# Optimization experiments

Hardware: AMD Instinct MI355X
Metric: run time of the kernel (lower is better)

The kernel has to match this reference:

```python
import jax, jax.numpy as jnp
import numpy as np

B, N, H = 16, 1024, 1024


def setup_inputs() -> dict:
    key = jax.random.key(0)
    ks = jax.random.split(key, 12)
    inv = 1.0 / np.sqrt(H)
    inp = {
        "x": jax.random.normal(ks[0], (B, N, H), jnp.float32),
        "atom_graph": jax.random.normal(ks[1], (B, N, N), jnp.float32),
        "variable_graph": jax.random.normal(ks[2], (B, N, N), jnp.float32),
        "Wq": jax.random.uniform(ks[3], (H, H), jnp.float32, -inv, inv),
        "bq": jax.random.uniform(ks[4], (H,), jnp.float32, -inv, inv),
        "Wk": jax.random.uniform(ks[5], (H, H), jnp.float32, -inv, inv),
        "bk": jax.random.uniform(ks[6], (H,), jnp.float32, -inv, inv),
        "Wv": jax.random.uniform(ks[7], (H, H), jnp.float32, -inv, inv),
        "bv": jax.random.uniform(ks[8], (H,), jnp.float32, -inv, inv),
        "predicate_pos": jax.random.randint(ks[9], (B, N), 0, 2, jnp.int32),
        "variable_tags": jax.random.randint(ks[10], (B, N), 0, 4, jnp.int32),
    }
    return inp


def _path_pool(h, predicate_pos):
    # h: [B,N,H]; predicate_pos: [B,N] in {0,1}
    b, n, d = h.shape
    i = jnp.arange(n)
    # pos[i-2] (value irrelevant for i<2, those branches handled explicitly)
    pp2 = jnp.pad(predicate_pos, ((0, 0), (2, 0)))[:, :n]  # [B,N]
    # window [s, e): i==0 -> [0,2); i==1 -> [0,3); pos[i-2]==1 -> [i,i+2); else [i-1,i+2)
    s = jnp.where(i < 2, 0, jnp.where(pp2 == 1, i, i - 1))  # [B,N]
    e = jnp.where(i == 0, 2, jnp.where(i == 1, 3, i + 2))    # [N]
    e = jnp.minimum(e, n)
    e = jnp.broadcast_to(e, (b, n))
    # prefix sums along node dim with a leading zero row -> windowed means via gather
    cs = jnp.concatenate([jnp.zeros((b, 1, d), h.dtype), jnp.cumsum(h, axis=1)], axis=1)  # [B,N+1,H]
    win_sum = (jnp.take_along_axis(cs, e[:, :, None], axis=1)
               - jnp.take_along_axis(cs, s[:, :, None], axis=1))  # [B,N,H]
    means = win_sum / (e - s)[:, :, None].astype(h.dtype)
    mask = (predicate_pos == 1).astype(h.dtype)  # [B,N]
    item = (means * mask[:, :, None]).sum(axis=1) / mask.sum(axis=1)[:, None]  # [B,H]
    return jnp.broadcast_to(item[:, None, :], (b, n, d))


def reference(x, atom_graph, variable_graph, Wq, bq, Wk, bk, Wv, bv,
              predicate_pos, variable_tags):
    scale = x.shape[-1] ** (-0.5)
    q = (x @ Wq.T + bq) * scale
    k = x @ Wk.T + bk
    v = x @ Wv.T + bv
    att = jnp.einsum("bnh,bmh->bnm", q, k) + atom_graph + variable_graph
    att = jax.nn.softmax(att, axis=-1)  # dropout is identity in eval
    h = jnp.einsum("bnm,bmh->bnh", att, v)
    return _path_pool(h, predicate_pos)
```

## Files before the change

kernel.cpp:

```cpp
#include <hip/hip_runtime.h>
#include <hip/hip_bf16.h>

#define BATCH 16
#define SEQ   1024
#define DIM   1024

typedef __attribute__((ext_vector_type(8))) short bf16x8;
typedef __attribute__((ext_vector_type(4))) float f32x4;
typedef __attribute__((ext_vector_type(4))) unsigned short us4;

__device__ __forceinline__ float bfu2f(unsigned short u) {
  union { unsigned int i; float f; } c; c.i = ((unsigned int)u) << 16; return c.f;
}
__device__ __forceinline__ unsigned short f2bfu(float f) {
  union { float f; unsigned int i; } c; c.f = f;
  return (unsigned short)((c.i + 0x7FFFu + ((c.i >> 16) & 1u)) >> 16);
}
__device__ __forceinline__ void async16(void* lds, const void* g) {
  __builtin_amdgcn_global_load_lds(
      (const __attribute__((address_space(1))) unsigned int*)g,
      (__attribute__((address_space(3))) unsigned int*)lds, 16, 0, 0);
}

__global__ void cast_f32_bf16(const float* __restrict__ in,
                              unsigned short* __restrict__ out, int n4) {
  int i = blockIdx.x * blockDim.x + threadIdx.x;
  if (i >= n4) return;
  f32x4 v = ((const f32x4*)in)[i];
  us4 o;
  o[0] = f2bfu(v[0]); o[1] = f2bfu(v[1]); o[2] = f2bfu(v[2]); o[3] = f2bfu(v[3]);
  ((us4*)out)[i] = o;
}

__global__ void castT_kernel(const float* __restrict__ Wq, const float* __restrict__ Wk,
                             unsigned short* __restrict__ WqT,
                             unsigned short* __restrict__ WkT) {
  const float* in = (blockIdx.z == 0) ? Wq : Wk;
  unsigned short* out = (blockIdx.z == 0) ? WqT : WkT;
  __shared__ float t[64][65];
  const int h0 = blockIdx.x * 64, i0 = blockIdx.y * 64;
  const int tid = threadIdx.x;
  const int sub = tid >> 4, c4 = tid & 15;
#pragma unroll
  for (int p = 0; p < 4; ++p) {
    const int row = p * 16 + sub;
    f32x4 v = *(const f32x4*)(in + (size_t)(h0 + row) * DIM + i0 + c4 * 4);
    t[row][c4 * 4 + 0] = v[0]; t[row][c4 * 4 + 1] = v[1];
    t[row][c4 * 4 + 2] = v[2]; t[row][c4 * 4 + 3] = v[3];
  }
  __syncthreads();
#pragma unroll
  for (int p = 0; p < 4; ++p) {
    const int orow = p * 16 + sub;
    us4 o;
    o[0] = f2bfu(t[c4 * 4 + 0][orow]);
    o[1] = f2bfu(t[c4 * 4 + 1][orow]);
    o[2] = f2bfu(t[c4 * 4 + 2][orow]);
    o[3] = f2bfu(t[c4 * 4 + 3][orow]);
    *(us4*)(out + (size_t)(i0 + orow) * DIM + h0 + c4 * 4) = o;
  }
}

__global__ void t12_kernel(const unsigned short* __restrict__ WqT,
                           const unsigned short* __restrict__ WkT,
                           const float* __restrict__ bq, const float* __restrict__ bk,
                           float* __restrict__ t1, float* __restrict__ t2) {
  const int y = blockIdx.y;
  const unsigned short* Wt = y ? WkT : WqT;
  const float* vec = y ? bq : bk;
  float* tout = y ? t2 : t1;
  const int wave = threadIdx.x >> 6, lane = threadIdx.x & 63;
  const int i = blockIdx.x * 4 + wave;
  const us4* wr = (const us4*)(Wt + (size_t)i * DIM);
  float s = 0.f;
#pragma unroll
  for (int t = 0; t < 4; ++t) {
    us4 w4 = wr[lane + 64 * t];
    f32x4 b4 = *(const f32x4*)(vec + (lane + 64 * t) * 4);
    s += bfu2f(w4[0]) * b4[0] + bfu2f(w4[1]) * b4[1] +
         bfu2f(w4[2]) * b4[2] + bfu2f(w4[3]) * b4[3];
  }
#pragma unroll
  for (int o = 32; o; o >>= 1) s += __shfl_down(s, o);
  if (lane == 0) tout[i] = s;
}

__global__ void ac_kernel(const unsigned short* __restrict__ xb,
                          const float* __restrict__ t1, const float* __restrict__ t2,
                          const float* __restrict__ bq, const float* __restrict__ bk,
                          float* __restrict__ a, float* __restrict__ c) {
  const float scale = 0.03125f;
  const int tid = threadIdx.x;
  const int wave = tid >> 6, lane = tid & 63;
  float dp = 0.f;
  for (int i = tid; i < DIM; i += 256) dp += bq[i] * bk[i];
#pragma unroll
  for (int o = 32; o; o >>= 1) dp += __shfl_down(dp, o);
  __shared__ float dred[4];
  if ((tid & 63) == 0) dred[tid >> 6] = dp;
  __syncthreads();
  const float d = dred[0] + dred[1] + dred[2] + dred[3];
  float t1r[16], t2r[16];
#pragma unroll
  for (int t = 0; t < 4; ++t) {
    f32x4 v1 = *(const f32x4*)(t1 + (lane + 64 * t) * 4);
    f32x4 v2 = *(const f32x4*)(t2 + (lane + 64 * t) * 4);
#pragma unroll
    for (int j = 0; j < 4; ++j) { t1r[t * 4 + j] = v1[j]; t2r[t * 4 + j] = v2[j]; }
  }
  for (int rr = 0; rr < 16; ++rr) {
    const int row = blockIdx.x * 64 + wave * 16 + rr;
    const us4* xr = (const us4*)(xb + (size_t)row * DIM);
    float sa = 0.f, sc = 0.f;
#pragma unroll
    for (int t = 0; t < 4; ++t) {
      us4 v = xr[lane + 64 * t];
#pragma unroll
      for (int j = 0; j < 4; ++j) {
        const float f = bfu2f(v[j]);
        sa += f * t1r[t * 4 + j];
        sc += f * t2r[t * 4 + j];
      }
    }
#pragma unroll
    for (int o = 32; o; o >>= 1) { sa += __shfl_down(sa, o); sc += __shfl_down(sc, o); }
    if (lane == 0) {
      a[row] = scale * (sa + d);
      c[row] = scale * sc;
    }
  }
}

__global__ void pathw_kernel(const int* __restrict__ pos, float* __restrict__ w,
                             float* __restrict__ denom, float* __restrict__ zbias) {
  const int b = blockIdx.x;
  __shared__ int ps[SEQ];
  __shared__ int mcnt;
  const int tid = threadIdx.x;
  if (tid == 0) mcnt = 0;
  __syncthreads();
  if (b == 0)
    for (int i = tid; i < DIM; i += 256) zbias[i] = 0.f;
  for (int i = tid; i < SEQ; i += 256) {
    ps[i] = pos[b * SEQ + i];
    denom[b * SEQ + i] = 0.f;
  }
  __syncthreads();
  int c = 0;
  for (int i = tid; i < SEQ; i += 256) c += ps[i];
  for (int o = 32; o; o >>= 1) c += __shfl_down(c, o);
  if ((tid & 63) == 0) atomicAdd(&mcnt, c);
  __syncthreads();
  const float invM = 1.0f / (float)mcnt;
  for (int j = tid; j < SEQ; j += 256) {
    float a = 0.f;
#pragma unroll
    for (int di = -1; di <= 1; ++di) {
      int i = j + di;
      if (i < 0 || i >= SEQ) continue;
      if (!ps[i]) continue;
      int s, e;
      if (i < 2) { s = 0; e = (i == 0) ? 2 : 3; }
      else { s = (ps[i - 2] == 1) ? i : (i - 1); e = i + 2; if (e > SEQ) e = SEQ; }
      if (s <= j && j < e) a += 1.0f / (float)(e - s);
    }
    w[b * SEQ + j] = a * invM;
  }
}

__global__ void proj_gemm(const unsigned short* __restrict__ A,
                          const unsigned short* __restrict__ W,
                          const float* __restrict__ bias, float alpha,
                          unsigned short* __restrict__ C, int M, int N, int K)
{
  __shared__ __align__(16) char smem[16896];
  unsigned short* As = (unsigned short*)smem;
  unsigned short* Bs = (unsigned short*)(smem + 8192);
  float* Sl = (float*)smem;
  const int tid = threadIdx.x;
  const int wave = tid >> 6, lane = tid & 63;
  const int lr = lane & 15, lg = lane >> 4;
  const int wr = wave >> 1, wc = wave & 1;
  const int m0 = blockIdx.x * 128, n0 = blockIdx.y * 128;
  const int off0 = tid * 16, off1 = 4096 + tid * 16;
  const int r0 = off0 >> 6, ke0 = (off0 >> 1) & 31;
  const int r1 = off1 >> 6, ke1 = (off1 >> 1) & 31;
  f32x4 acc[4][4] = {};
  for (int kk = 0; kk < K; kk += 32) {
    async16((char*)As + off0, A + (size_t)(m0 + r0) * K + kk + ke0);
    async16((char*)As + off1, A + (size_t)(m0 + r1) * K + kk + ke1);
    async16((char*)Bs + off0, W + (size_t)(n0 + r0) * K + kk + ke0);
    async16((char*)Bs + off1, W + (size_t)(n0 + r1) * K + kk + ke1);
    __syncthreads();
    bf16x8 af[4], bfv[4];
#pragma unroll
    for (int i = 0; i < 4; ++i) {
      af[i]  = *(const bf16x8*)((const char*)As + ((wr * 64 + i * 16 + lr) << 6) + (lg << 4));
      bfv[i] = *(const bf16x8*)((const char*)Bs + ((wc * 64 + i * 16 + lr) << 6) + (lg << 4));
    }
#pragma unroll
    for (int i = 0; i < 4; ++i)
#pragma unroll
      for (int j = 0; j < 4; ++j)
        acc[i][j] = __builtin_amdgcn_mfma_f32_16x16x32_bf16(af[i], bfv[j], acc[i][j], 0, 0, 0);
    __syncthreads();
  }
#pragma unroll
  for (int p = 0; p < 4; ++p) {
    __syncthreads();
    if (wr == (p >> 1)) {
      const int ibase = (p & 1) * 2;
#pragma unroll
      for (int ii = 0; ii < 2; ++ii) {
        const int i = ibase + ii;
#pragma unroll
        for (int j = 0; j < 4; ++j)
#pragma unroll
          for (int r = 0; r < 4; ++r)
            Sl[(ii * 16 + lg * 4 + r) * 132 + wc * 64 + j * 16 + lr] = acc[i][j][r];
      }
    }
    __syncthreads();
#pragma unroll
    for (int it = 0; it < 4; ++it) {
      const int v = tid + it * 256;
      const int lrow = v >> 5, c4 = v & 31;
      const int grow = m0 + p * 32 + lrow;
      const int col = n0 + c4 * 4;
      const f32x4 s4 = *(const f32x4*)(&Sl[lrow * 132 + c4 * 4]);
      const f32x4 b4 = *(const f32x4*)(bias + col);
      us4 o;
      o[0] = f2bfu((s4[0] + b4[0]) * alpha);
      o[1] = f2bfu((s4[1] + b4[1]) * alpha);
      o[2] = f2bfu((s4[2] + b4[2]) * alpha);
      o[3] = f2bfu((s4[3] + b4[3]) * alpha);
      *(us4*)(C + (size_t)grow * N + col) = o;
    }
  }
}

__global__ void qk_exp_kernel(const unsigned short* __restrict__ z,
                              const unsigned short* __restrict__ xb,
                              const float* __restrict__ ag,
                              const float* __restrict__ vg,
                              const float* __restrict__ av,
                              const float* __restrict__ cv,
                              unsigned short* __restrict__ E,
                              float* __restrict__ denom)
{
  __shared__ __align__(16) char smem[16896];
  unsigned short* As = (unsigned short*)smem;
  unsigned short* Bs = (unsigned short*)(smem + 8192);
  float* Sl = (float*)smem;
  const int b = blockIdx.z;
  const unsigned short* Aq = z + ((size_t)b << 20);
  const unsigned short* Bk = xb + ((size_t)b << 20);
  const int tid = threadIdx.x;
  const int wave = tid >> 6, lane = tid & 63;
  const int lr = lane & 15, lg = lane >> 4;
  const int wr = wave >> 1, wc = wave & 1;
  const int m0 = blockIdx.y * 128, n0 = blockIdx.x * 128;
  const int off0 = tid * 16, off1 = 4096 + tid * 16;
  const int r0 = off0 >> 6, ke0 = (off0 >> 1) & 31;
  const int r1 = off1 >> 6, ke1 = (off1 >> 1) & 31;
  f32x4 acc[4][4] = {};
  for (int kk = 0; kk < DIM; kk += 32) {
    async16((char*)As + off0, Aq + (size_t)(m0 + r0) * DIM + kk + ke0);
    async16((char*)As + off1, Aq + (size_t)(m0 + r1) * DIM + kk + ke1);
    async16((char*)Bs + off0, Bk + (size_t)(n0 + r0) * DIM + kk + ke0);
    async16((char*)Bs + off1, Bk + (size_t)(n0 + r1) * DIM + kk + ke1);
    __syncthreads();
    bf16x8 af[4], bfv[4];
#pragma unroll
    for (int i = 0; i < 4; ++i) {
      af[i]  = *(const bf16x8*)((const char*)As + ((wr * 64 + i * 16 + lr) << 6) + (lg << 4));
      bfv[i] = *(const bf16x8*)((const char*)Bs + ((wc * 64 + i * 16 + lr) << 6) + (lg << 4));
    }
#pragma unroll
    for (int i = 0; i < 4; ++i)
#pragma unroll
      for (int j = 0; j < 4; ++j)
        acc[i][j] = __builtin_amdgcn_mfma_f32_16x16x32_bf16(af[i], bfv[j], acc[i][j], 0, 0, 0);
    __syncthreads();
  }
  const float* agb = ag + ((size_t)b << 20);
  const float* vgb = vg + ((size_t)b << 20);
  unsigned short* Eb = E + ((size_t)b << 20);
  float* dnb = denom + b * SEQ;
  const float* avb = av + b * SEQ;
  const float* cvb = cv + b * SEQ;
#pragma unroll
  for (int p = 0; p < 4; ++p) {
    __syncthreads();
    if (wr == (p >> 1)) {
      const int ibase = (p & 1) * 2;
#pragma unroll
      for (int ii = 0; ii < 2; ++ii) {
        const int i = ibase + ii;
#pragma unroll
        for (int j = 0; j < 4; ++j)
#pragma unroll
          for (int r = 0; r < 4; ++r)
            Sl[(ii * 16 + lg * 4 + r) * 132 + wc * 64 + j * 16 + lr] = acc[i][j][r];
      }
    }
    __syncthreads();
#pragma unroll
    for (int it = 0; it < 4; ++it) {
      const int v = tid + it * 256;
      const int lrow = v >> 5, c4 = v & 31;
      const int grow = m0 + p * 32 + lrow;
      const size_t base = (size_t)grow * SEQ + n0 + c4 * 4;
      const f32x4 a4 = *(const f32x4*)(agb + base);
      const f32x4 g4 = *(const f32x4*)(vgb + base);
      const f32x4 c4v = *(const f32x4*)(cvb + n0 + c4 * 4);
      const float arow = avb[grow];
      const f32x4 s4 = *(const f32x4*)(&Sl[lrow * 132 + c4 * 4]);
      const float e0 = __expf(s4[0] + a4[0] + g4[0] + arow + c4v[0]);
      const float e1 = __expf(s4[1] + a4[1] + g4[1] + arow + c4v[1]);
      const float e2 = __expf(s4[2] + a4[2] + g4[2] + arow + c4v[2]);
      const float e3 = __expf(s4[3] + a4[3] + g4[3] + arow + c4v[3]);
      us4 o;
      o[0] = f2bfu(e0); o[1] = f2bfu(e1); o[2] = f2bfu(e2); o[3] = f2bfu(e3);
      *(us4*)(Eb + base) = o;
      float rs = e0 + e1 + e2 + e3;
#pragma unroll
      for (int o2 = 16; o2; o2 >>= 1) rs += __shfl_down(rs, o2, 32);
      if ((tid & 31) == 0) atomicAdd(&dnb[grow], rs);
    }
  }
}

__global__ void wcolsum_part(const unsigned short* __restrict__ Mt,
                             const float* __restrict__ wv,
                             const float* __restrict__ dv,
                             float* __restrict__ part) {
  const int b = blockIdx.z;
  const int nc = blockIdx.y;
  const int m = blockIdx.x * 256 + threadIdx.x;
  __shared__ float c[128];
  const int tid = threadIdx.x;
  if (tid < 128) {
    const int n = nc * 128 + tid;
    float cvw = wv[b * SEQ + n];
    if (dv) cvw /= dv[b * SEQ + n];
    c[tid] = cvw;
  }
  __syncthreads();
  const unsigned short* p = Mt + ((size_t)b << 20) + ((size_t)(nc * 128) << 10) + m;
  float acc = 0.f;
#pragma unroll 8
  for (int n = 0; n < 128; ++n) acc += c[n] * bfu2f(p[(size_t)n << 10]);
  part[(size_t)((b * 8 + nc) << 10) + m] = acc;
}

__global__ void wcolsum_reduce(const float* __restrict__ part, float* __restrict__ out) {
  const int b = blockIdx.y;
  const int m = blockIdx.x * 256 + threadIdx.x;
  float s = 0.f;
#pragma unroll
  for (int nc = 0; nc < 8; ++nc) s += part[(size_t)((b * 8 + nc) << 10) + m];
  out[b * SEQ + m] = s;
}

__global__ void item_kernel(const float* __restrict__ y, const float* __restrict__ u,
                            const unsigned short* __restrict__ Wvb,
                            const float* __restrict__ bv, float* __restrict__ item) {
  const int b = blockIdx.x;
  const int hblk = blockIdx.y;
  __shared__ float ys[DIM];
  __shared__ float sred[4];
  const int tid = threadIdx.x;
  float part = 0.f;
  for (int i = tid; i < DIM; i += 256) { ys[i] = y[b * DIM + i]; part += u[b * SEQ + i]; }
  for (int o = 32; o; o >>= 1) part += __shfl_down(part, o);
  if ((tid & 63) == 0) sred[tid >> 6] = part;
  __syncthreads();
  const float su = sred[0] + sred[1] + sred[2] + sred[3];
  const int wave = tid >> 6, lane = tid & 63;
  const int h = hblk * 4 + wave;
  const us4* wrow = (const us4*)(Wvb + (size_t)h * DIM);
  float acc = 0.f;
#pragma unroll
  for (int t = 0; t < 4; ++t) {
    us4 v = wrow[t * 64 + lane];
    const int d0 = (t * 64 + lane) * 4;
    acc += ys[d0] * bfu2f(v[0]) + ys[d0 + 1] * bfu2f(v[1]) +
           ys[d0 + 2] * bfu2f(v[2]) + ys[d0 + 3] * bfu2f(v[3]);
  }
  for (int o = 32; o; o >>= 1) acc += __shfl_down(acc, o);
  if (lane == 0) item[b * DIM + h] = acc + su * bv[h];
}

__global__ void bcast_kernel(const float* __restrict__ item, float* __restrict__ out) {
  const int b = blockIdx.y;
  const int n = blockIdx.x;
  const f32x4* src = (const f32x4*)(item + b * DIM);
  f32x4* dst = (f32x4*)(out + (((size_t)b * SEQ + n) << 10));
  dst[threadIdx.x] = src[threadIdx.x];
}

extern "C" void kernel_launch(void* const* d_in, const int* in_sizes, int n_in,
                              void* d_out, int out_size, void* d_ws, size_t ws_size,
                              hipStream_t stream) {
  const float* x    = (const float*)d_in[0];
  const float* ag   = (const float*)d_in[1];
  const float* vgr  = (const float*)d_in[2];
  const float* Wq   = (const float*)d_in[3];
  const float* bq   = (const float*)d_in[4];
  const float* Wk   = (const float*)d_in[5];
  const float* bk   = (const float*)d_in[6];
  const float* Wv   = (const float*)d_in[7];
  const float* bv   = (const float*)d_in[8];
  const int*   pos  = (const int*)d_in[9];
  float* out = (float*)d_out;

  char* ws = (char*)d_ws;
  size_t off = 0;
  auto alloc = [&](size_t bytes) { void* p = ws + off; off += (bytes + 255) & ~(size_t)255; return p; };
  const size_t BNH = (size_t)BATCH * SEQ * DIM;
  unsigned short* xb   = (unsigned short*)alloc(BNH * 2);
  unsigned short* zb   = (unsigned short*)alloc(BNH * 2);
  unsigned short* E    = (unsigned short*)alloc(BNH * 2);
  unsigned short* WqT  = (unsigned short*)alloc((size_t)DIM * DIM * 2);
  unsigned short* WkT  = (unsigned short*)alloc((size_t)DIM * DIM * 2);
  unsigned short* Wvb  = (unsigned short*)alloc((size_t)DIM * DIM * 2);
  unsigned short* Hb   = (unsigned short*)alloc((size_t)DIM * DIM * 2);
  float* w     = (float*)alloc((size_t)BATCH * SEQ * 4);
  float* denom = (float*)alloc((size_t)BATCH * SEQ * 4);
  float* u     = (float*)alloc((size_t)BATCH * SEQ * 4);
  float* av    = (float*)alloc((size_t)BATCH * SEQ * 4);
  float* cvv   = (float*)alloc((size_t)BATCH * SEQ * 4);
  float* t1    = (float*)alloc((size_t)DIM * 4);
  float* t2    = (float*)alloc((size_t)DIM * 4);
  float* zbias = (float*)alloc((size_t)DIM * 4);
  float* y     = (float*)alloc((size_t)BATCH * DIM * 4);
  float* item  = (float*)alloc((size_t)BATCH * DIM * 4);
  float* part  = (float*)alloc((size_t)BATCH * 8 * SEQ * 4);

  const float scale = 0.03125f;

  cast_f32_bf16<<<(int)(BNH / 4 / 256), 256, 0, stream>>>(x, xb, (int)(BNH / 4));
  cast_f32_bf16<<<DIM * DIM / 4 / 256, 256, 0, stream>>>(Wv, Wvb, DIM * DIM / 4);
  castT_kernel<<<dim3(16, 16, 2), 256, 0, stream>>>(Wq, Wk, WqT, WkT);

  pathw_kernel<<<BATCH, 256, 0, stream>>>(pos, w, denom, zbias);

  t12_kernel<<<dim3(256, 2), 256, 0, stream>>>(WqT, WkT, bq, bk, t1, t2);
  ac_kernel<<<256, 256, 0, stream>>>(xb, t1, t2, bq, bk, av, cvv);

  proj_gemm<<<dim3(8, 8), 256, 0, stream>>>(WkT, WqT, zbias, scale, Hb, DIM, DIM, DIM);

  proj_gemm<<<dim3(128, 8), 256, 0, stream>>>(xb, Hb, zbias, 1.0f, zb,
                                              BATCH * SEQ, DIM, DIM);

  qk_exp_kernel<<<dim3(8, 8, BATCH), 256, 0, stream>>>(zb, xb, ag, vgr, av, cvv, E, denom);

  wcolsum_part<<<dim3(4, 8, BATCH), 256, 0, stream>>>(E, w, denom, part);
  wcolsum_reduce<<<dim3(4, BATCH), 256, 0, stream>>>(part, u);

  wcolsum_part<<<dim3(4, 8, BATCH), 256, 0, stream>>>(xb, u, nullptr, part);
  wcolsum_reduce<<<dim3(4, BATCH), 256, 0, stream>>>(part, y);

  item_kernel<<<dim3(BATCH, 256), 256, 0, stream>>>(y, u, Wvb, bv, item);

  bcast_kernel<<<dim3(SEQ, BATCH), 256, 0, stream>>>(item, out);
}
```

Measured before the change: 237.5 us.

## Overlap exp epilogue with second tile GEMM and fuse small reduction kernels

The QK-exp kernel now computes two adjacent 128-column tiles per block. The exp/bias epilogue of the first tile is interleaved into the k-loop of the second tile's MFMA GEMM, so global loads of the attention-graph inputs overlap matrix work, with launch bounds set for two blocks per CU. The x and Wv casts are merged into one launch, and one wcolsum_reduce is removed by having the consumer kernels sum the 8 partials themselves. This trades a larger register footprint (two accumulator sets) and half as many blocks for fewer launches and better overlap.

```diff
diff --git a/kernel.cpp b/kernel.cpp
--- a/kernel.cpp
+++ b/kernel.cpp
@@ -22,14 +22,17 @@
       (__attribute__((address_space(3))) unsigned int*)lds, 16, 0, 0);
 }
 
-__global__ void cast_f32_bf16(const float* __restrict__ in,
-                              unsigned short* __restrict__ out, int n4) {
+__global__ void cast_xw_kernel(const float* __restrict__ x, const float* __restrict__ Wv,
+                               unsigned short* __restrict__ xb,
+                               unsigned short* __restrict__ Wvb, int x4) {
   int i = blockIdx.x * blockDim.x + threadIdx.x;
-  if (i >= n4) return;
-  f32x4 v = ((const f32x4*)in)[i];
+  const float* in; unsigned short* out; int j;
+  if (i < x4) { in = x; out = xb; j = i; }
+  else { in = Wv; out = Wvb; j = i - x4; }
+  f32x4 v = ((const f32x4*)in)[j];
   us4 o;
   o[0] = f2bfu(v[0]); o[1] = f2bfu(v[1]); o[2] = f2bfu(v[2]); o[3] = f2bfu(v[3]);
-  ((us4*)out)[i] = o;
+  ((us4*)out)[j] = o;
 }
 
 __global__ void castT_kernel(const float* __restrict__ Wq, const float* __restrict__ Wk,
@@ -239,19 +242,19 @@
   }
 }
 
-__global__ void qk_exp_kernel(const unsigned short* __restrict__ z,
-                              const unsigned short* __restrict__ xb,
-                              const float* __restrict__ ag,
-                              const float* __restrict__ vg,
-                              const float* __restrict__ av,
-                              const float* __restrict__ cv,
-                              unsigned short* __restrict__ E,
-                              float* __restrict__ denom)
+__global__ __launch_bounds__(256, 2)
+void qk_exp_kernel(const unsigned short* __restrict__ z,
+                   const unsigned short* __restrict__ xb,
+                   const float* __restrict__ ag,
+                   const float* __restrict__ vg,
+                   const float* __restrict__ av,
+                   const float* __restrict__ cv,
+                   unsigned short* __restrict__ E,
+                   float* __restrict__ denom)
 {
-  __shared__ __align__(16) char smem[16896];
-  unsigned short* As = (unsigned short*)smem;
-  unsigned short* Bs = (unsigned short*)(smem + 8192);
-  float* Sl = (float*)smem;
+  __shared__ __align__(16) unsigned short As[128 * 32];
+  __shared__ __align__(16) unsigned short Bs[128 * 32];
+  __shared__ __align__(16) float Sl[32 * 132];
   const int b = blockIdx.z;
   const unsigned short* Aq = z + ((size_t)b << 20);
   const unsigned short* Bk = xb + ((size_t)b << 20);
@@ -259,39 +262,65 @@
   const int wave = tid >> 6, lane = tid & 63;
   const int lr = lane & 15, lg = lane >> 4;
   const int wr = wave >> 1, wc = wave & 1;
-  const int m0 = blockIdx.y * 128, n0 = blockIdx.x * 128;
+  const int m0 = blockIdx.y * 128;
+  const int n0a = blockIdx.x * 256, n0b = n0a + 128;
   const int off0 = tid * 16, off1 = 4096 + tid * 16;
   const int r0 = off0 >> 6, ke0 = (off0 >> 1) & 31;
   const int r1 = off1 >> 6, ke1 = (off1 >> 1) & 31;
-  f32x4 acc[4][4] = {};
-  for (int kk = 0; kk < DIM; kk += 32) {
-    async16((char*)As + off0, Aq + (size_t)(m0 + r0) * DIM + kk + ke0);
-    async16((char*)As + off1, Aq + (size_t)(m0 + r1) * DIM + kk + ke1);
-    async16((char*)Bs + off0, Bk + (size_t)(n0 + r0) * DIM + kk + ke0);
-    async16((char*)Bs + off1, Bk + (size_t)(n0 + r1) * DIM + kk + ke1);
-    __syncthreads();
-    bf16x8 af[4], bfv[4];
-#pragma unroll
-    for (int i = 0; i < 4; ++i) {
-      af[i]  = *(const bf16x8*)((const char*)As + ((wr * 64 + i * 16 + lr) << 6) + (lg << 4));
-      bfv[i] = *(const bf16x8*)((const char*)Bs + ((wc * 64 + i * 16 + lr) << 6) + (lg << 4));
-    }
-#pragma unroll
-    for (int i = 0; i < 4; ++i)
-#pragma unroll
-      for (int j = 0; j < 4; ++j)
-        acc[i][j] = __builtin_amdgcn_mfma_f32_16x16x32_bf16(af[i], bfv[j], acc[i][j], 0, 0, 0);
-    __syncthreads();
-  }
   const float* agb = ag + ((size_t)b << 20);
   const float* vgb = vg + ((size_t)b << 20);
   unsigned short* Eb = E + ((size_t)b << 20);
   float* dnb = denom + b * SEQ;
   const float* avb = av + b * SEQ;
   const float* cvb = cv + b * SEQ;
+
+  auto chunk = [&](int p, int it, int nb) {
+    const int v = tid + it * 256;
+    const int lrow = v >> 5, c4 = v & 31;
+    const int grow = m0 + p * 32 + lrow;
+    const size_t base = (size_t)grow * SEQ + nb + c4 * 4;
+    const f32x4 a4 = *(const f32x4*)(agb + base);
+    const f32x4 g4 = *(const f32x4*)(vgb + base);
+    const f32x4 c4v = *(const f32x4*)(cvb + nb + c4 * 4);
+    const float arow = avb[grow];
+    const f32x4 s4 = *(const f32x4*)(&Sl[lrow * 132 + c4 * 4]);
+    const float e0 = __expf(s4[0] + a4[0] + g4[0] + arow + c4v[0]);
+    const float e1 = __expf(s4[1] + a4[1] + g4[1] + arow + c4v[1]);
+    const float e2 = __expf(s4[2] + a4[2] + g4[2] + arow + c4v[2]);
+    const float e3 = __expf(s4[3] + a4[3] + g4[3] + arow + c4v[3]);
+    us4 o;
+    o[0] = f2bfu(e0); o[1] = f2bfu(e1); o[2] = f2bfu(e2); o[3] = f2bfu(e3);
+    *(us4*)(Eb + base) = o;
+    float rs = e0 + e1 + e2 + e3;
+#pragma unroll
+    for (int o2 = 16; o2; o2 >>= 1) rs += __shfl_down(rs, o2, 32);
+    if ((tid & 31) == 0) atomicAdd(&dnb[grow], rs);
+  };
+
+  f32x4 acc1[4][4] = {}, acc2[4][4] = {};
+
+  for (int kk = 0; kk < DIM; kk += 32) {
+    async16((char*)As + off0, Aq + (size_t)(m0 + r0) * DIM + kk + ke0);
+    async16((char*)As + off1, Aq + (size_t)(m0 + r1) * DIM + kk + ke1);
+    async16((char*)Bs + off0, Bk + (size_t)(n0a + r0) * DIM + kk + ke0);
+    async16((char*)Bs + off1, Bk + (size_t)(n0a + r1) * DIM + kk + ke1);
+    __syncthreads();
+    bf16x8 af[4], bfv[4];
+#pragma unroll
+    for (int i = 0; i < 4; ++i) {
+      af[i]  = *(const bf16x8*)((const char*)As + ((wr * 64 + i * 16 + lr) << 6) + (lg << 4));
+      bfv[i] = *(const bf16x8*)((const char*)Bs + ((wc * 64 + i * 16 + lr) << 6) + (lg << 4));
+    }
+#pragma unroll
+    for (int i = 0; i < 4; ++i)
+#pragma unroll
+      for (int j = 0; j < 4; ++j)
+        acc1[i][j] = __builtin_amdgcn_mfma_f32_16x16x32_bf16(af[i], bfv[j], acc1[i][j], 0, 0, 0);
+    __syncthreads();
+  }
+
 #pragma unroll
   for (int p = 0; p < 4; ++p) {
-    __syncthreads();
     if (wr == (p >> 1)) {
       const int ibase = (p & 1) * 2;
 #pragma unroll
@@ -301,39 +330,59 @@
         for (int j = 0; j < 4; ++j)
 #pragma unroll
           for (int r = 0; r < 4; ++r)
-            Sl[(ii * 16 + lg * 4 + r) * 132 + wc * 64 + j * 16 + lr] = acc[i][j][r];
+            Sl[(ii * 16 + lg * 4 + r) * 132 + wc * 64 + j * 16 + lr] = acc1[i][j][r];
       }
     }
     __syncthreads();
 #pragma unroll
-    for (int it = 0; it < 4; ++it) {
-      const int v = tid + it * 256;
-      const int lrow = v >> 5, c4 = v & 31;
-      const int grow = m0 + p * 32 + lrow;
-      const size_t base = (size_t)grow * SEQ + n0 + c4 * 4;
-      const f32x4 a4 = *(const f32x4*)(agb + base);
-      const f32x4 g4 = *(const f32x4*)(vgb + base);
-      const f32x4 c4v = *(const f32x4*)(cvb + n0 + c4 * 4);
-      const float arow = avb[grow];
-      const f32x4 s4 = *(const f32x4*)(&Sl[lrow * 132 + c4 * 4]);
-      const float e0 = __expf(s4[0] + a4[0] + g4[0] + arow + c4v[0]);
-      const float e1 = __expf(s4[1] + a4[1] + g4[1] + arow + c4v[1]);
-      const float e2 = __expf(s4[2] + a4[2] + g4[2] + arow + c4v[2]);
-      const float e3 = __expf(s4[3] + a4[3] + g4[3] + arow + c4v[3]);
-      us4 o;
-      o[0] = f2bfu(e0); o[1] = f2bfu(e1); o[2] = f2bfu(e2); o[3] = f2bfu(e3);
-      *(us4*)(Eb + base) = o;
-      float rs = e0 + e1 + e2 + e3;
-#pragma unroll
-      for (int o2 = 16; o2; o2 >>= 1) rs += __shfl_down(rs, o2, 32);
-      if ((tid & 31) == 0) atomicAdd(&dnb[grow], rs);
-    }
+    for (int ks = 0; ks < 8; ++ks) {
+      const int kk = (p * 8 + ks) * 32;
+      async16((char*)As + off0, Aq + (size_t)(m0 + r0) * DIM + kk + ke0);
+      async16((char*)As + off1, Aq + (size_t)(m0 + r1) * DIM + kk + ke1);
+      async16((char*)Bs + off0, Bk + (size_t)(n0b + r0) * DIM + kk + ke0);
+      async16((char*)Bs + off1, Bk + (size_t)(n0b + r1) * DIM + kk + ke1);
+      __syncthreads();
+      bf16x8 af[4], bfv[4];
+#pragma unroll
+      for (int i = 0; i < 4; ++i) {
+        af[i]  = *(const bf16x8*)((const char*)As + ((wr * 64 + i * 16 + lr) << 6) + (lg << 4));
+        bfv[i] = *(const bf16x8*)((const char*)Bs + ((wc * 64 + i * 16 + lr) << 6) + (lg << 4));
+      }
+      if ((ks & 1) == 0) chunk(p, ks >> 1, n0a);
+#pragma unroll
+      for (int i = 0; i < 4; ++i)
+#pragma unroll
+        for (int j = 0; j < 4; ++j)
+          acc2[i][j] = __builtin_amdgcn_mfma_f32_16x16x32_bf16(af[i], bfv[j], acc2[i][j], 0, 0, 0);
+      __syncthreads();
+    }
+  }
+
+#pragma unroll
+  for (int p = 0; p < 4; ++p) {
+    if (wr == (p >> 1)) {
+      const int ibase = (p & 1) * 2;
+#pragma unroll
+      for (int ii = 0; ii < 2; ++ii) {
+        const int i = ibase + ii;
+#pragma unroll
+        for (int j = 0; j < 4; ++j)
+#pragma unroll
+          for (int r = 0; r < 4; ++r)
+            Sl[(ii * 16 + lg * 4 + r) * 132 + wc * 64 + j * 16 + lr] = acc2[i][j][r];
+      }
+    }
+    __syncthreads();
+#pragma unroll
+    for (int it = 0; it < 4; ++it) chunk(p, it, n0b);
+    __syncthreads();
   }
 }
 
 __global__ void wcolsum_part(const unsigned short* __restrict__ Mt,
                              const float* __restrict__ wv,
                              const float* __restrict__ dv,
+                             const float* __restrict__ pin,
                              float* __restrict__ part) {
   const int b = blockIdx.z;
   const int nc = blockIdx.y;
@@ -342,8 +391,15 @@
   const int tid = threadIdx.x;
   if (tid < 128) {
     const int n = nc * 128 + tid;
-    float cvw = wv[b * SEQ + n];
-    if (dv) cvw /= dv[b * SEQ + n];
+    float cvw;
+    if (pin) {
+      cvw = 0.f;
+#pragma unroll
+      for (int j = 0; j < 8; ++j) cvw += pin[(size_t)((b * 8 + j) << 10) + n];
+    } else {
+      cvw = wv[b * SEQ + n];
+      if (dv) cvw /= dv[b * SEQ + n];
+    }
     c[tid] = cvw;
   }
   __syncthreads();
@@ -363,7 +419,7 @@
   out[b * SEQ + m] = s;
 }
 
-__global__ void item_kernel(const float* __restrict__ y, const float* __restrict__ u,
+__global__ void item_kernel(const float* __restrict__ y, const float* __restrict__ part1,
                             const unsigned short* __restrict__ Wvb,
                             const float* __restrict__ bv, float* __restrict__ item) {
   const int b = blockIdx.x;
@@ -372,7 +428,8 @@
   __shared__ float sred[4];
   const int tid = threadIdx.x;
   float part = 0.f;
-  for (int i = tid; i < DIM; i += 256) { ys[i] = y[b * DIM + i]; part += u[b * SEQ + i]; }
+  for (int i = tid; i < DIM; i += 256) ys[i] = y[b * DIM + i];
+  for (int i = tid; i < 8 * SEQ; i += 256) part += part1[(size_t)(b * 8) * SEQ + i];
   for (int o = 32; o; o >>= 1) part += __shfl_down(part, o);
   if ((tid & 63) == 0) sred[tid >> 6] = part;
   __syncthreads();
@@ -428,7 +485,6 @@
   unsigned short* Hb   = (unsigned short*)alloc((size_t)DIM * DIM * 2);
   float* w     = (float*)alloc((size_t)BATCH * SEQ * 4);
   float* denom = (float*)alloc((size_t)BATCH * SEQ * 4);
-  float* u     = (float*)alloc((size_t)BATCH * SEQ * 4);
   float* av    = (float*)alloc((size_t)BATCH * SEQ * 4);
   float* cvv   = (float*)alloc((size_t)BATCH * SEQ * 4);
   float* t1    = (float*)alloc((size_t)DIM * 4);
@@ -436,12 +492,13 @@
   float* zbias = (float*)alloc((size_t)DIM * 4);
   float* y     = (float*)alloc((size_t)BATCH * DIM * 4);
   float* item  = (float*)alloc((size_t)BATCH * DIM * 4);
-  float* part  = (float*)alloc((size_t)BATCH * 8 * SEQ * 4);
+  float* part1 = (float*)alloc((size_t)BATCH * 8 * SEQ * 4);
+  float* part2 = (float*)alloc((size_t)BATCH * 8 * SEQ * 4);
 
   const float scale = 0.03125f;
-
-  cast_f32_bf16<<<(int)(BNH / 4 / 256), 256, 0, stream>>>(x, xb, (int)(BNH / 4));
-  cast_f32_bf16<<<DIM * DIM / 4 / 256, 256, 0, stream>>>(Wv, Wvb, DIM * DIM / 4);
+  const int x4 = (int)(BNH / 4);
+
+  cast_xw_kernel<<<(x4 + DIM * DIM / 4) / 256, 256, 0, stream>>>(x, Wv, xb, Wvb, x4);
   castT_kernel<<<dim3(16, 16, 2), 256, 0, stream>>>(Wq, Wk, WqT, WkT);
 
   pathw_kernel<<<BATCH, 256, 0, stream>>>(pos, w, denom, zbias);
@@ -454,15 +511,14 @@
   proj_gemm<<<dim3(128, 8), 256, 0, stream>>>(xb, Hb, zbias, 1.0f, zb,
                                               BATCH * SEQ, DIM, DIM);
 
-  qk_exp_kernel<<<dim3(8, 8, BATCH), 256, 0, stream>>>(zb, xb, ag, vgr, av, cvv, E, denom);
-
-  wcolsum_part<<<dim3(4, 8, BATCH), 256, 0, stream>>>(E, w, denom, part);
-  wcolsum_reduce<<<dim3(4, BATCH), 256, 0, stream>>>(part, u);
-
-  wcolsum_part<<<dim3(4, 8, BATCH), 256, 0, stream>>>(xb, u, nullptr, part);
-  wcolsum_reduce<<<dim3(4, BATCH), 256, 0, stream>>>(part, y);
-
-  item_kernel<<<dim3(BATCH, 256), 256, 0, stream>>>(y, u, Wvb, bv, item);
+  qk_exp_kernel<<<dim3(4, 8, BATCH), 256, 0, stream>>>(zb, xb, ag, vgr, av, cvv, E, denom);
+
+  wcolsum_part<<<dim3(4, 8, BATCH), 256, 0, stream>>>(E, w, denom, nullptr, part1);
+
+  wcolsum_part<<<dim3(4, 8, BATCH), 256, 0, stream>>>(xb, nullptr, nullptr, part1, part2);
+  wcolsum_reduce<<<dim3(4, BATCH), 256, 0, stream>>>(part2, y);
+
+  item_kernel<<<dim3(BATCH, 256), 256, 0, stream>>>(y, part1, Wvb, bv, item);
 
   bcast_kernel<<<dim3(SEQ, BATCH), 256, 0, stream>>>(item, out);
 }
```

Result: slower. 259.4 us (+9.2%).

## Remap GEMM block order across XCDs and fold small reduction launches

Applied to the files above, without the earlier changes.

Merges the two f32-to-bf16 cast launches into one kernel. Remaps the flat block index in proj_gemm and qk_exp_kernel so consecutive tiles that share operands land on the same XCD, aiming to improve L2 reuse. Drops the first wcolsum_reduce launch by having the second wcolsum_part and item_kernel sum the 8 partials directly. This adds a little redundant partial summation per block in exchange for fewer launches.

```diff
diff --git a/kernel.cpp b/kernel.cpp
--- a/kernel.cpp
+++ b/kernel.cpp
@@ -22,14 +22,17 @@
       (__attribute__((address_space(3))) unsigned int*)lds, 16, 0, 0);
 }
 
-__global__ void cast_f32_bf16(const float* __restrict__ in,
-                              unsigned short* __restrict__ out, int n4) {
+__global__ void cast_xw_kernel(const float* __restrict__ x, const float* __restrict__ Wv,
+                               unsigned short* __restrict__ xb,
+                               unsigned short* __restrict__ Wvb, int x4) {
   int i = blockIdx.x * blockDim.x + threadIdx.x;
-  if (i >= n4) return;
-  f32x4 v = ((const f32x4*)in)[i];
+  const float* in; unsigned short* out; int j;
+  if (i < x4) { in = x; out = xb; j = i; }
+  else { in = Wv; out = Wvb; j = i - x4; }
+  f32x4 v = ((const f32x4*)in)[j];
   us4 o;
   o[0] = f2bfu(v[0]); o[1] = f2bfu(v[1]); o[2] = f2bfu(v[2]); o[3] = f2bfu(v[3]);
-  ((us4*)out)[i] = o;
+  ((us4*)out)[j] = o;
 }
 
 __global__ void castT_kernel(const float* __restrict__ Wq, const float* __restrict__ Wk,
@@ -181,7 +184,11 @@
   const int wave = tid >> 6, lane = tid & 63;
   const int lr = lane & 15, lg = lane >> 4;
   const int wr = wave >> 1, wc = wave & 1;
-  const int m0 = blockIdx.x * 128, n0 = blockIdx.y * 128;
+  const int flat = blockIdx.x + gridDim.x * blockIdx.y;
+  const int q8 = (gridDim.x * gridDim.y) >> 3;
+  const int t = (flat & 7) * q8 + (flat >> 3);
+  const int m0 = (t / gridDim.y) * 128;
+  const int n0 = (t % gridDim.y) * 128;
   const int off0 = tid * 16, off1 = 4096 + tid * 16;
   const int r0 = off0 >> 6, ke0 = (off0 >> 1) & 31;
   const int r1 = off1 >> 6, ke1 = (off1 >> 1) & 31;
@@ -252,14 +259,17 @@
   unsigned short* As = (unsigned short*)smem;
   unsigned short* Bs = (unsigned short*)(smem + 8192);
   float* Sl = (float*)smem;
-  const int b = blockIdx.z;
+  const int flat = blockIdx.x + 8 * blockIdx.y + 64 * blockIdx.z;
+  const int t = (flat & 7) * 128 + (flat >> 3);
+  const int b = t >> 6;
+  const int m0 = (t & 7) * 128;
+  const int n0 = ((t >> 3) & 7) * 128;
   const unsigned short* Aq = z + ((size_t)b << 20);
   const unsigned short* Bk = xb + ((size_t)b << 20);
   const int tid = threadIdx.x;
   const int wave = tid >> 6, lane = tid & 63;
   const int lr = lane & 15, lg = lane >> 4;
   const int wr = wave >> 1, wc = wave & 1;
-  const int m0 = blockIdx.y * 128, n0 = blockIdx.x * 128;
   const int off0 = tid * 16, off1 = 4096 + tid * 16;
   const int r0 = off0 >> 6, ke0 = (off0 >> 1) & 31;
   const int r1 = off1 >> 6, ke1 = (off1 >> 1) & 31;
@@ -334,6 +344,7 @@
 __global__ void wcolsum_part(const unsigned short* __restrict__ Mt,
                              const float* __restrict__ wv,
                              const float* __restrict__ dv,
+                             const float* __restrict__ pin,
                              float* __restrict__ part) {
   const int b = blockIdx.z;
   const int nc = blockIdx.y;
@@ -342,8 +353,15 @@
   const int tid = threadIdx.x;
   if (tid < 128) {
     const int n = nc * 128 + tid;
-    float cvw = wv[b * SEQ + n];
-    if (dv) cvw /= dv[b * SEQ + n];
+    float cvw;
+    if (pin) {
+      cvw = 0.f;
+#pragma unroll
+      for (int j = 0; j < 8; ++j) cvw += pin[(size_t)((b * 8 + j) << 10) + n];
+    } else {
+      cvw = wv[b * SEQ + n];
+      if (dv) cvw /= dv[b * SEQ + n];
+    }
     c[tid] = cvw;
   }
   __syncthreads();
@@ -363,7 +381,7 @@
   out[b * SEQ + m] = s;
 }
 
-__global__ void item_kernel(const float* __restrict__ y, const float* __restrict__ u,
+__global__ void item_kernel(const float* __restrict__ y, const float* __restrict__ part1,
                             const unsigned short* __restrict__ Wvb,
                             const float* __restrict__ bv, float* __restrict__ item) {
   const int b = blockIdx.x;
@@ -372,7 +390,8 @@
   __shared__ float sred[4];
   const int tid = threadIdx.x;
   float part = 0.f;
-  for (int i = tid; i < DIM; i += 256) { ys[i] = y[b * DIM + i]; part += u[b * SEQ + i]; }
+  for (int i = tid; i < DIM; i += 256) ys[i] = y[b * DIM + i];
+  for (int i = tid; i < 8 * SEQ; i += 256) part += part1[(size_t)(b * 8) * SEQ + i];
   for (int o = 32; o; o >>= 1) part += __shfl_down(part, o);
   if ((tid & 63) == 0) sred[tid >> 6] = part;
   __syncthreads();
@@ -428,7 +447,6 @@
   unsigned short* Hb   = (unsigned short*)alloc((size_t)DIM * DIM * 2);
   float* w     = (float*)alloc((size_t)BATCH * SEQ * 4);
   float* denom = (float*)alloc((size_t)BATCH * SEQ * 4);
-  float* u     = (float*)alloc((size_t)BATCH * SEQ * 4);
   float* av    = (float*)alloc((size_t)BATCH * SEQ * 4);
   float* cvv   = (float*)alloc((size_t)BATCH * SEQ * 4);
   float* t1    = (float*)alloc((size_t)DIM * 4);
@@ -436,12 +454,13 @@
   float* zbias = (float*)alloc((size_t)DIM * 4);
   float* y     = (float*)alloc((size_t)BATCH * DIM * 4);
   float* item  = (float*)alloc((size_t)BATCH * DIM * 4);
-  float* part  = (float*)alloc((size_t)BATCH * 8 * SEQ * 4);
+  float* part1 = (float*)alloc((size_t)BATCH * 8 * SEQ * 4);
+  float* part2 = (float*)alloc((size_t)BATCH * 8 * SEQ * 4);
 
   const float scale = 0.03125f;
-
-  cast_f32_bf16<<<(int)(BNH / 4 / 256), 256, 0, stream>>>(x, xb, (int)(BNH / 4));
-  cast_f32_bf16<<<DIM * DIM / 4 / 256, 256, 0, stream>>>(Wv, Wvb, DIM * DIM / 4);
+  const int x4 = (int)(BNH / 4);
+
+  cast_xw_kernel<<<(x4 + DIM * DIM / 4) / 256, 256, 0, stream>>>(x, Wv, xb, Wvb, x4);
   castT_kernel<<<dim3(16, 16, 2), 256, 0, stream>>>(Wq, Wk, WqT, WkT);
 
   pathw_kernel<<<BATCH, 256, 0, stream>>>(pos, w, denom, zbias);
@@ -456,13 +475,12 @@
 
   qk_exp_kernel<<<dim3(8, 8, BATCH), 256, 0, stream>>>(zb, xb, ag, vgr, av, cvv, E, denom);
 
-  wcolsum_part<<<dim3(4, 8, BATCH), 256, 0, stream>>>(E, w, denom, part);
-  wcolsum_reduce<<<dim3(4, BATCH), 256, 0, stream>>>(part, u);
-
-  wcolsum_part<<<dim3(4, 8, BATCH), 256, 0, stream>>>(xb, u, nullptr, part);
-  wcolsum_reduce<<<dim3(4, BATCH), 256, 0, stream>>>(part, y);
-
-  item_kernel<<<dim3(BATCH, 256), 256, 0, stream>>>(y, u, Wvb, bv, item);
+  wcolsum_part<<<dim3(4, 8, BATCH), 256, 0, stream>>>(E, w, denom, nullptr, part1);
+
+  wcolsum_part<<<dim3(4, 8, BATCH), 256, 0, stream>>>(xb, nullptr, nullptr, part1, part2);
+  wcolsum_reduce<<<dim3(4, BATCH), 256, 0, stream>>>(part2, y);
+
+  item_kernel<<<dim3(BATCH, 256), 256, 0, stream>>>(y, part1, Wvb, bv, item);
 
   bcast_kernel<<<dim3(SEQ, BATCH), 256, 0, stream>>>(item, out);
 }
```

New measurement: 232.1 us. 1.02x faster.
